# Kernel tuning notes

Hardware: AMD Instinct MI355X
Metric: run time of the kernel (lower is better)

Reference implementation:

```python
import jax, jax.numpy as jnp
import numpy as np

B, N, D, OUT = 4, 4096, 2048, 2048
E, RANK, TOP_K = 8, 16, 2
ALPHA = 16.0
SCALING = ALPHA / RANK


def setup_inputs() -> dict:
    key = jax.random.key(0)
    k1, k2, k3, k4 = jax.random.split(key, 4)
    x = jax.random.normal(k1, (B, N, D), dtype=jnp.float32)
    weight = jax.random.normal(k2, (OUT, D), dtype=jnp.float32) * (1.0 / np.sqrt(D))
    router_w = jax.random.normal(k3, (E, D), dtype=jnp.float32) * 0.02
    experts_A = jax.random.normal(k4, (E, D, RANK), dtype=jnp.float32) * (1.0 / np.sqrt(RANK))
    # experts_B is zero-initialized in the module; use small random values so the
    # LoRA branch contributes non-trivially to the output for kernel testing.
    experts_B = jax.random.normal(jax.random.fold_in(key, 5), (E, RANK, OUT), dtype=jnp.float32) * 0.02
    return {"x": x, "weight": weight, "router_w": router_w,
            "experts_A": experts_A, "experts_B": experts_B}


def reference(x, weight, router_w, experts_A, experts_B):
    # base = F.linear(x, weight)  (no bias)
    base = jnp.einsum('bnd,od->bno', x, weight)
    # router logits: x @ W_r^T -> (B, N, E)
    logits = jnp.einsum('bnd,ed->bne', x, router_w)
    # top-k sparse routing: keep top-k logits, set rest to -inf, softmax
    topk_vals, topk_idx = jax.lax.top_k(logits, TOP_K)  # (B,N,K)
    keep = jax.nn.one_hot(topk_idx, E, dtype=jnp.bool_).any(axis=-2)  # (B,N,E)
    masked = jnp.where(keep, logits, -jnp.inf)
    router_weights = jax.nn.softmax(masked, axis=-1)  # (B,N,E)
    # per-expert low-rank down/up projection, weighted by router
    lora_down = jnp.einsum('bnd,edr->bner', x, experts_A)  # (B,N,E,rank)
    weighted = lora_down * router_weights[..., None]
    moe_out = jnp.einsum('bner,erd->bnd', weighted, experts_B)  # (B,N,OUT)
    return base + SCALING * moe_out
```

## Files before the change

kernel.cpp:

```cpp
#include <hip/hip_runtime.h>
#include <stdint.h>

#define D_DIM 2048
#define OUT_DIM 2048
#define NTOK 16384
#define SCALING 1.0f
#define NT32 68

typedef unsigned short u16;
typedef __attribute__((ext_vector_type(8))) short s16x8;
typedef __attribute__((ext_vector_type(4))) float f32x4;

#define WZ_OFF  0u
#define AZ_OFF  8388608u
#define BZ_OFF  8912896u
#define CZ_OFF  9437184u
#define XB_OFF  14155776u
#define WS_BIG   81264640u

__device__ inline u16 f2bf(float f) {
  union { float f; uint32_t u; } v; v.f = f;
  uint32_t u = v.u;
  u += 0x7FFFu + ((u >> 16) & 1u);
  return (u16)(u >> 16);
}

__device__ inline int swz32(int c, int row) {
  return (c & ~31) | (((((c >> 3) & 3) ^ ((row >> 1) & 3))) << 3) | (c & 7);
}

#define GLDS(gp, lp) __builtin_amdgcn_global_load_lds( \
    (const __attribute__((address_space(1))) void*)(gp), \
    (__attribute__((address_space(3))) void*)(lp), 16, 0, 0)

__global__ __launch_bounds__(256) void k_prep(const float* __restrict__ W,
                                              const float* __restrict__ A,
                                              const float* __restrict__ Bf,
                                              u16* __restrict__ Wz,
                                              u16* __restrict__ Az,
                                              u16* __restrict__ Bz) {
  int bid = blockIdx.x;
  if (bid < 4096) {
    int idx = bid * 256 + threadIdx.x;
    int o  = idx >> 9;
    int k0 = (idx & 511) * 4;
    const float4 v = *(const float4*)&W[(size_t)o * D_DIM + k0];
    int dst = swz32(k0, o);
    uint32_t p0 = (uint32_t)f2bf(v.x) | ((uint32_t)f2bf(v.y) << 16);
    uint32_t p1 = (uint32_t)f2bf(v.z) | ((uint32_t)f2bf(v.w) << 16);
    *(uint2*)&Wz[(size_t)o * D_DIM + dst] = make_uint2(p0, p1);
    return;
  }
  if (bid < 5120) {
    int idx = (bid - 4096) * 256 + threadIdx.x;
    float v = A[idx];
    int r = idx & 15;
    int d = (idx >> 4) & 2047;
    int e = idx >> 15;
    int er = e * 16 + r;
    Az[(size_t)er * D_DIM + swz32(d, er)] = f2bf(v);
    return;
  }
  {
    int idx = (bid - 5120) * 256 + threadIdx.x;
    float v = Bf[idx];
    int er = idx >> 11;
    int o  = idx & 2047;
    Bz[(size_t)o * 128 + swz32(er, o)] = f2bf(v);
  }
}

__global__ __launch_bounds__(256) void k_router_lora(
    const float* __restrict__ x, const float* __restrict__ rw,
    const u16* __restrict__ Az, u16* __restrict__ xb, u16* __restrict__ Cz) {
  __shared__ u16 Axl[2][64 * 64];
  __shared__ u16 Bzl[2][128 * 64];
  __shared__ float w8s[64 * 8];
  int tid = threadIdx.x, lane = tid & 63, wid = tid >> 6;
  int t0 = blockIdx.x * 64;
  const int l15 = lane & 15;

  f32x4 acc[8];
#pragma unroll
  for (int n = 0; n < 8; ++n) acc[n] = (f32x4){0.f, 0.f, 0.f, 0.f};
  float lgp[4][8];
#pragma unroll
  for (int i = 0; i < 4; ++i)
#pragma unroll
    for (int e = 0; e < 8; ++e) lgp[i][e] = 0.f;

  auto stage = [&](int kc, int buf) {
    bool real = (kc <= 31);
    if (!real) kc = 31;
    const int c4 = (tid & 15) * 4;
    float4 rv[8];
    if (real) {
#pragma unroll
      for (int e = 0; e < 8; ++e)
        rv[e] = *(const float4*)&rw[(size_t)e * D_DIM + kc * 64 + c4];
    }
#pragma unroll
    for (int i = 0; i < 4; ++i) {
      int row = i * 16 + (tid >> 4);
      float4 v = *(const float4*)&x[(size_t)(t0 + row) * D_DIM + kc * 64 + c4];
      uint32_t p0 = (uint32_t)f2bf(v.x) | ((uint32_t)f2bf(v.y) << 16);
      uint32_t p1 = (uint32_t)f2bf(v.z) | ((uint32_t)f2bf(v.w) << 16);
      *(uint2*)&xb[(size_t)(t0 + row) * D_DIM + swz32(kc * 64 + c4, row)] =
          make_uint2(p0, p1);
      *(uint2*)&Axl[buf][row * 64 + swz32(c4, row)] = make_uint2(p0, p1);
      if (real) {
#pragma unroll
        for (int e = 0; e < 8; ++e) {
          lgp[i][e] = fmaf(v.x, rv[e].x, lgp[i][e]);
          lgp[i][e] = fmaf(v.y, rv[e].y, lgp[i][e]);
          lgp[i][e] = fmaf(v.z, rv[e].z, lgp[i][e]);
          lgp[i][e] = fmaf(v.w, rv[e].w, lgp[i][e]);
        }
      }
    }
#pragma unroll
    for (int i = 0; i < 4; ++i) {
      const u16* g = Az + (size_t)(i * 32 + (tid >> 3)) * D_DIM + kc * 64 + (tid & 7) * 8;
      GLDS(g, &Bzl[buf][0] + i * 2048 + tid * 8);
    }
  };

  stage(0, 0);
  asm volatile("s_waitcnt vmcnt(0) lgkmcnt(0)" ::: "memory");
  __builtin_amdgcn_s_barrier();

  for (int kc = 0; kc < 32; ++kc) {
    int cur = kc & 1;
    stage(kc + 1, cur ^ 1);
    const int g = (lane >> 4) ^ ((l15 >> 1) & 3);
#pragma unroll
    for (int kk = 0; kk < 2; ++kk) {
      s16x8 af = *(const s16x8*)&Axl[cur][(wid * 16 + l15) * 64 + kk * 32 + g * 8];
#pragma unroll
      for (int nf = 0; nf < 8; ++nf) {
        s16x8 bf = *(const s16x8*)&Bzl[cur][(nf * 16 + l15) * 64 + kk * 32 + g * 8];
        acc[nf] = __builtin_amdgcn_mfma_f32_16x16x32_bf16(af, bf, acc[nf], 0, 0, 0);
      }
    }
    asm volatile("s_waitcnt vmcnt(0) lgkmcnt(0)" ::: "memory");
    __builtin_amdgcn_s_barrier();
  }

#pragma unroll
  for (int i = 0; i < 4; ++i) {
#pragma unroll
    for (int e = 0; e < 8; ++e) {
      float v = lgp[i][e];
      v += __shfl_xor(v, 1, 64);
      v += __shfl_xor(v, 2, 64);
      v += __shfl_xor(v, 4, 64);
      v += __shfl_xor(v, 8, 64);
      lgp[i][e] = v;
    }
    float l0 = lgp[i][0]; int i0 = 0;
#pragma unroll
    for (int e = 1; e < 8; ++e) if (lgp[i][e] > l0) { l0 = lgp[i][e]; i0 = e; }
    float l1 = -3e38f; int i1 = 0;
#pragma unroll
    for (int e = 0; e < 8; ++e) if (e != i0 && lgp[i][e] > l1) { l1 = lgp[i][e]; i1 = e; }
    float e1 = expf(l1 - l0);
    float inv = 1.f / (1.f + e1);
    if (l15 < 8) {
      int row = i * 16 + (tid >> 4);
      w8s[row * 8 + l15] =
          (l15 == i0) ? inv * SCALING : (l15 == i1) ? e1 * inv * SCALING : 0.f;
    }
  }
  __syncthreads();

#pragma unroll
  for (int q = 0; q < 4; ++q) {
    int rl = wid * 16 + (lane >> 4) * 4 + q;
#pragma unroll
    for (int nf = 0; nf < 8; ++nf) {
      float v = acc[nf][q] * w8s[rl * 8 + nf];
      int er = nf * 16 + l15;
      Cz[(size_t)(t0 + rl) * 128 + swz32(er, rl)] = f2bf(v);
    }
  }
}

__global__ __launch_bounds__(512, 2) void k_main32(const u16* __restrict__ xb,
                                                   const u16* __restrict__ Wz,
                                                   const u16* __restrict__ Cz,
                                                   const u16* __restrict__ Bz,
                                                   float* __restrict__ out) {
  __shared__ u16 AL[4][8192];
  __shared__ u16 BL[4][8192];
  const int tid = threadIdx.x, lane = tid & 63;
  const int wid = tid >> 6, wm = wid >> 2, wn = wid & 3;
  int bid = blockIdx.x;
  int swz = (bid & 7) * 64 + (bid >> 3);
  int mt = swz >> 3, nt = swz & 7;
  int t0 = mt * 256, o0 = nt * 256;
  const int l15 = lane & 15;
  const int gA = (lane >> 4) ^ ((l15 >> 1) & 3);
  const int aoff = (wm * 128 + l15) * 32 + gA * 8;
  const int boff = (wn * 64 + l15) * 32 + gA * 8;
  const int srow = tid >> 2, sc8 = (tid & 3) * 8;

  f32x4 acc[8][4];
#pragma unroll
  for (int m = 0; m < 8; ++m)
#pragma unroll
    for (int n = 0; n < 4; ++n) acc[m][n] = (f32x4){0.f, 0.f, 0.f, 0.f};
  s16x8 aA[8], bA[4], aB[8], bB[4];

  auto stg = [&](int t, int bufi) {
    if (t > NT32 - 1) t = NT32 - 1;
    const u16 *sa, *sb; int lda, ldb, ca;
    if (t < 64) { sa = xb; lda = D_DIM; sb = Wz; ldb = D_DIM; ca = t * 32; }
    else        { sa = Cz; lda = 128;   sb = Bz; ldb = 128;   ca = (t - 64) * 32; }
#pragma unroll
    for (int i = 0; i < 2; ++i) {
      const u16* g = sa + (size_t)(t0 + i * 128 + srow) * lda + ca + sc8;
      GLDS(g, &AL[bufi][0] + i * 4096 + tid * 8);
    }
#pragma unroll
    for (int i = 0; i < 2; ++i) {
      const u16* g = sb + (size_t)(o0 + i * 128 + srow) * ldb + ca + sc8;
      GLDS(g, &BL[bufi][0] + i * 4096 + tid * 8);
    }
  };

#define RD(av, bv, bufi) do {                                           \
    const u16* ap_ = &AL[bufi][aoff];                                   \
    const u16* bp_ = &BL[bufi][boff];                                   \
    _Pragma("unroll") for (int i_ = 0; i_ < 8; ++i_)                    \
      av[i_] = *(const s16x8*)(ap_ + i_ * 512);                         \
    _Pragma("unroll") for (int j_ = 0; j_ < 4; ++j_)                    \
      bv[j_] = *(const s16x8*)(bp_ + j_ * 512);                         \
  } while (0)

#define MM(av, bv) do {                                                 \
    __builtin_amdgcn_s_setprio(1);                                      \
    _Pragma("unroll") for (int mf_ = 0; mf_ < 8; ++mf_)                 \
      _Pragma("unroll") for (int nf_ = 0; nf_ < 4; ++nf_)               \
        acc[mf_][nf_] = __builtin_amdgcn_mfma_f32_16x16x32_bf16(        \
            av[mf_], bv[nf_], acc[mf_][nf_], 0, 0, 0);                  \
    __builtin_amdgcn_s_setprio(0);                                      \
  } while (0)

  stg(0, 0); stg(1, 1); stg(2, 2);
  asm volatile("s_waitcnt vmcnt(4)" ::: "memory");
  __builtin_amdgcn_s_barrier();
  RD(aA, bA, 0);

  for (int jj = 0; jj < NT32; jj += 2) {
    RD(aB, bB, (jj + 1) & 3);
    MM(aA, bA);
    stg(jj + 3, (jj + 3) & 3);
    asm volatile("s_waitcnt vmcnt(4)" ::: "memory");
    __builtin_amdgcn_s_barrier();
    RD(aA, bA, (jj + 2) & 3);
    MM(aB, bB);
    stg(jj + 4, (jj + 4) & 3);
    asm volatile("s_waitcnt vmcnt(4)" ::: "memory");
    __builtin_amdgcn_s_barrier();
  }
  asm volatile("s_waitcnt vmcnt(0) lgkmcnt(0)" ::: "memory");
#undef RD
#undef MM

#pragma unroll
  for (int mf = 0; mf < 8; ++mf)
#pragma unroll
    for (int q = 0; q < 4; ++q) {
      int row = t0 + wm * 128 + mf * 16 + (lane >> 4) * 4 + q;
#pragma unroll
      for (int nf = 0; nf < 4; ++nf) {
        int col = o0 + wn * 64 + nf * 16 + l15;
        out[(size_t)row * OUT_DIM + col] = acc[mf][nf][q];
      }
    }
}

extern "C" void kernel_launch(void* const* d_in, const int* in_sizes, int n_in,
                              void* d_out, int out_size, void* d_ws, size_t ws_size,
                              hipStream_t stream) {
  const float* x  = (const float*)d_in[0];
  const float* W  = (const float*)d_in[1];
  const float* rw = (const float*)d_in[2];
  const float* eA = (const float*)d_in[3];
  const float* eB = (const float*)d_in[4];
  float* out = (float*)d_out;
  char* ws = (char*)d_ws;
  if (ws_size < WS_BIG) return;

  u16* Wz = (u16*)(ws + WZ_OFF);
  u16* Az = (u16*)(ws + AZ_OFF);
  u16* Bz = (u16*)(ws + BZ_OFF);
  u16* Cz = (u16*)(ws + CZ_OFF);
  u16* xb = (u16*)(ws + XB_OFF);

  k_prep<<<6144, 256, 0, stream>>>(W, eA, eB, Wz, Az, Bz);
  k_router_lora<<<256, 256, 0, stream>>>(x, rw, Az, xb, Cz);
  k_main32<<<512, 512, 0, stream>>>(xb, Wz, Cz, Bz, out);
}
```

Before: 225.5 us.

## Overlap weight conversion with router kernel and software-pipeline x loads

```diff
diff --git a/kernel.cpp b/kernel.cpp
--- a/kernel.cpp
+++ b/kernel.cpp
@@ -33,52 +33,50 @@
     (const __attribute__((address_space(1))) void*)(gp), \
     (__attribute__((address_space(3))) void*)(lp), 16, 0, 0)
 
-__global__ __launch_bounds__(256) void k_prep(const float* __restrict__ W,
-                                              const float* __restrict__ A,
-                                              const float* __restrict__ Bf,
-                                              u16* __restrict__ Wz,
-                                              u16* __restrict__ Az,
-                                              u16* __restrict__ Bz) {
-  int bid = blockIdx.x;
-  if (bid < 4096) {
-    int idx = bid * 256 + threadIdx.x;
-    int o  = idx >> 9;
-    int k0 = (idx & 511) * 4;
-    const float4 v = *(const float4*)&W[(size_t)o * D_DIM + k0];
-    int dst = swz32(k0, o);
-    uint32_t p0 = (uint32_t)f2bf(v.x) | ((uint32_t)f2bf(v.y) << 16);
-    uint32_t p1 = (uint32_t)f2bf(v.z) | ((uint32_t)f2bf(v.w) << 16);
-    *(uint2*)&Wz[(size_t)o * D_DIM + dst] = make_uint2(p0, p1);
-    return;
-  }
-  if (bid < 5120) {
-    int idx = (bid - 4096) * 256 + threadIdx.x;
-    float v = A[idx];
-    int r = idx & 15;
-    int d = (idx >> 4) & 2047;
-    int e = idx >> 15;
-    int er = e * 16 + r;
-    Az[(size_t)er * D_DIM + swz32(d, er)] = f2bf(v);
-    return;
-  }
-  {
-    int idx = (bid - 5120) * 256 + threadIdx.x;
-    float v = Bf[idx];
-    int er = idx >> 11;
-    int o  = idx & 2047;
-    Bz[(size_t)o * 128 + swz32(er, o)] = f2bf(v);
-  }
+__global__ __launch_bounds__(256) void k_prep_a(const float* __restrict__ A,
+                                                u16* __restrict__ Az) {
+  int idx = blockIdx.x * 256 + threadIdx.x;
+  float v = A[idx];
+  int r = idx & 15;
+  int d = (idx >> 4) & 2047;
+  int e = idx >> 15;
+  int er = e * 16 + r;
+  Az[(size_t)er * D_DIM + swz32(d, er)] = f2bf(v);
 }
 
 __global__ __launch_bounds__(256) void k_router_lora(
     const float* __restrict__ x, const float* __restrict__ rw,
-    const u16* __restrict__ Az, u16* __restrict__ xb, u16* __restrict__ Cz) {
+    const float* __restrict__ W, const float* __restrict__ Bf,
+    const u16* __restrict__ Az, u16* __restrict__ xb, u16* __restrict__ Cz,
+    u16* __restrict__ Wz, u16* __restrict__ Bz) {
+  int bid = blockIdx.x;
+  if (bid >= 256) {
+    if (bid < 4352) {
+      int idx = (bid - 256) * 256 + threadIdx.x;
+      int o  = idx >> 9;
+      int k0 = (idx & 511) * 4;
+      const float4 v = *(const float4*)&W[(size_t)o * D_DIM + k0];
+      int dst = swz32(k0, o);
+      uint32_t p0 = (uint32_t)f2bf(v.x) | ((uint32_t)f2bf(v.y) << 16);
+      uint32_t p1 = (uint32_t)f2bf(v.z) | ((uint32_t)f2bf(v.w) << 16);
+      *(uint2*)&Wz[(size_t)o * D_DIM + dst] = make_uint2(p0, p1);
+    } else {
+      int idx = (bid - 4352) * 256 + threadIdx.x;
+      float v = Bf[idx];
+      int er = idx >> 11;
+      int o  = idx & 2047;
+      Bz[(size_t)o * 128 + swz32(er, o)] = f2bf(v);
+    }
+    return;
+  }
   __shared__ u16 Axl[2][64 * 64];
   __shared__ u16 Bzl[2][128 * 64];
   __shared__ float w8s[64 * 8];
   int tid = threadIdx.x, lane = tid & 63, wid = tid >> 6;
-  int t0 = blockIdx.x * 64;
+  int t0 = bid * 64;
   const int l15 = lane & 15;
+  const int c4 = (tid & 15) * 4;
+  const int rbase = tid >> 4;
 
   f32x4 acc[8];
 #pragma unroll
@@ -89,34 +87,37 @@
 #pragma unroll
     for (int e = 0; e < 8; ++e) lgp[i][e] = 0.f;
 
-  auto stage = [&](int kc, int buf) {
+  float4 xn[4];
+  auto ldx = [&](int kc) {
+    if (kc > 31) kc = 31;
+#pragma unroll
+    for (int i = 0; i < 4; ++i)
+      xn[i] = *(const float4*)&x[(size_t)(t0 + i * 16 + rbase) * D_DIM + kc * 64 + c4];
+  };
+  auto use = [&](int kc, int buf) {
     bool real = (kc <= 31);
     if (!real) kc = 31;
-    const int c4 = (tid & 15) * 4;
-    float4 rv[8];
     if (real) {
 #pragma unroll
-      for (int e = 0; e < 8; ++e)
-        rv[e] = *(const float4*)&rw[(size_t)e * D_DIM + kc * 64 + c4];
+      for (int e = 0; e < 8; ++e) {
+        float4 rv = *(const float4*)&rw[(size_t)e * D_DIM + kc * 64 + c4];
+#pragma unroll
+        for (int i = 0; i < 4; ++i) {
+          lgp[i][e] = fmaf(xn[i].x, rv.x, lgp[i][e]);
+          lgp[i][e] = fmaf(xn[i].y, rv.y, lgp[i][e]);
+          lgp[i][e] = fmaf(xn[i].z, rv.z, lgp[i][e]);
+          lgp[i][e] = fmaf(xn[i].w, rv.w, lgp[i][e]);
+        }
+      }
     }
 #pragma unroll
     for (int i = 0; i < 4; ++i) {
-      int row = i * 16 + (tid >> 4);
-      float4 v = *(const float4*)&x[(size_t)(t0 + row) * D_DIM + kc * 64 + c4];
-      uint32_t p0 = (uint32_t)f2bf(v.x) | ((uint32_t)f2bf(v.y) << 16);
-      uint32_t p1 = (uint32_t)f2bf(v.z) | ((uint32_t)f2bf(v.w) << 16);
+      int row = i * 16 + rbase;
+      uint32_t p0 = (uint32_t)f2bf(xn[i].x) | ((uint32_t)f2bf(xn[i].y) << 16);
+      uint32_t p1 = (uint32_t)f2bf(xn[i].z) | ((uint32_t)f2bf(xn[i].w) << 16);
       *(uint2*)&xb[(size_t)(t0 + row) * D_DIM + swz32(kc * 64 + c4, row)] =
           make_uint2(p0, p1);
       *(uint2*)&Axl[buf][row * 64 + swz32(c4, row)] = make_uint2(p0, p1);
-      if (real) {
-#pragma unroll
-        for (int e = 0; e < 8; ++e) {
-          lgp[i][e] = fmaf(v.x, rv[e].x, lgp[i][e]);
-          lgp[i][e] = fmaf(v.y, rv[e].y, lgp[i][e]);
-          lgp[i][e] = fmaf(v.z, rv[e].z, lgp[i][e]);
-          lgp[i][e] = fmaf(v.w, rv[e].w, lgp[i][e]);
-        }
-      }
     }
 #pragma unroll
     for (int i = 0; i < 4; ++i) {
@@ -125,14 +126,15 @@
     }
   };
 
-  stage(0, 0);
+  ldx(0);
+  use(0, 0);
   asm volatile("s_waitcnt vmcnt(0) lgkmcnt(0)" ::: "memory");
   __builtin_amdgcn_s_barrier();
 
+  const int g = (lane >> 4) ^ ((l15 >> 1) & 3);
   for (int kc = 0; kc < 32; ++kc) {
     int cur = kc & 1;
-    stage(kc + 1, cur ^ 1);
-    const int g = (lane >> 4) ^ ((l15 >> 1) & 3);
+    ldx(kc + 1);
 #pragma unroll
     for (int kk = 0; kk < 2; ++kk) {
       s16x8 af = *(const s16x8*)&Axl[cur][(wid * 16 + l15) * 64 + kk * 32 + g * 8];
@@ -142,6 +144,7 @@
         acc[nf] = __builtin_amdgcn_mfma_f32_16x16x32_bf16(af, bf, acc[nf], 0, 0, 0);
       }
     }
+    use(kc + 1, cur ^ 1);
     asm volatile("s_waitcnt vmcnt(0) lgkmcnt(0)" ::: "memory");
     __builtin_amdgcn_s_barrier();
   }
@@ -166,7 +169,7 @@
     float e1 = expf(l1 - l0);
     float inv = 1.f / (1.f + e1);
     if (l15 < 8) {
-      int row = i * 16 + (tid >> 4);
+      int row = i * 16 + rbase;
       w8s[row * 8 + l15] =
           (l15 == i0) ? inv * SCALING : (l15 == i1) ? e1 * inv * SCALING : 0.f;
     }
@@ -238,12 +241,10 @@
   } while (0)
 
 #define MM(av, bv) do {                                                 \
-    __builtin_amdgcn_s_setprio(1);                                      \
     _Pragma("unroll") for (int mf_ = 0; mf_ < 8; ++mf_)                 \
       _Pragma("unroll") for (int nf_ = 0; nf_ < 4; ++nf_)               \
         acc[mf_][nf_] = __builtin_amdgcn_mfma_f32_16x16x32_bf16(        \
             av[mf_], bv[nf_], acc[mf_][nf_], 0, 0, 0);                  \
-    __builtin_amdgcn_s_setprio(0);                                      \
   } while (0)
 
   stg(0, 0); stg(1, 1); stg(2, 2);
@@ -298,7 +299,7 @@
   u16* Cz = (u16*)(ws + CZ_OFF);
   u16* xb = (u16*)(ws + XB_OFF);
 
-  k_prep<<<6144, 256, 0, stream>>>(W, eA, eB, Wz, Az, Bz);
-  k_router_lora<<<256, 256, 0, stream>>>(x, rw, Az, xb, Cz);
+  k_prep_a<<<1024, 256, 0, stream>>>(eA, Az);
+  k_router_lora<<<5376, 256, 0, stream>>>(x, rw, W, eB, Az, xb, Cz, Wz, Bz);
   k_main32<<<512, 512, 0, stream>>>(xb, Wz, Cz, Bz, out);
 }
```

After: 223.9 us, median of 4. About the same (-0.7%).
